# Performance work log

Hardware: AMD Instinct MI355X
Metric: run time of the kernel (lower is better)

The kernel has to match this reference:

```python
import jax, jax.numpy as jnp
import numpy as np

B, S, E, D, V, H, NL = 16, 1024, 64, 256, 10000, 8, 3
HD = D // H


def _ln(x, g, b):
    m = jnp.mean(x, -1, keepdims=True)
    v = jnp.mean((x - m) ** 2, -1, keepdims=True)
    return (x - m) / jnp.sqrt(v + 1e-5) * g + b


def _mha(q_in, kv_in, in_w, in_b, out_w, out_b, causal):
    # torch nn.MultiheadAttention with packed in_proj [3D, D]
    d = q_in.shape[-1]
    q = q_in @ in_w[:d].T + in_b[:d]
    k = kv_in @ in_w[d:2 * d].T + in_b[d:2 * d]
    v = kv_in @ in_w[2 * d:].T + in_b[2 * d:]
    sp = lambda t: t.reshape(t.shape[0], t.shape[1], H, HD).transpose(0, 2, 1, 3)
    q, k, v = sp(q), sp(k), sp(v)
    s = jnp.einsum('bhqd,bhkd->bhqk', q, k) / jnp.float32(np.sqrt(HD))
    if causal:
        L = s.shape[-1]
        s = jnp.where(jnp.tril(jnp.ones((L, L), bool)), s, jnp.float32(-1e30))
    a = jax.nn.softmax(s, -1)
    o = jnp.einsum('bhqk,bhkd->bhqd', a, v).transpose(0, 2, 1, 3).reshape(q_in.shape[0], -1, d)
    return o @ out_w.T + out_b


def setup_inputs() -> dict:
    key = jax.random.key(0)
    ks = iter(jax.random.split(key, 40))
    n = lambda *sh: jax.random.normal(next(ks), sh, jnp.float32) * 0.05
    d = dict(
        tractovka=n(B, E), context=n(B, E), card=n(B, E),
        enc_w=n(3, D, E), enc_b=n(3, D),
        enc_ln_g=jnp.ones((3, D), jnp.float32), enc_ln_b=jnp.zeros((3, D), jnp.float32),
        fusion_w=n(D, 3 * D), fusion_b=n(D),
        fusion_ln_g=jnp.ones(D, jnp.float32), fusion_ln_b=jnp.zeros(D, jnp.float32),
        tok_emb=n(V, D), pos_emb=n(1024, D),
        sa_in_w=n(NL, 3 * D, D), sa_in_b=n(NL, 3 * D), sa_out_w=n(NL, D, D), sa_out_b=n(NL, D),
        ca_in_w=n(NL, 3 * D, D), ca_in_b=n(NL, 3 * D), ca_out_w=n(NL, D, D), ca_out_b=n(NL, D),
        ln1_g=jnp.ones((NL, D), jnp.float32), ln1_b=jnp.zeros((NL, D), jnp.float32),
        ln2_g=jnp.ones((NL, D), jnp.float32), ln2_b=jnp.zeros((NL, D), jnp.float32),
        ln3_g=jnp.ones((NL, D), jnp.float32), ln3_b=jnp.zeros((NL, D), jnp.float32),
        ffn_w1=n(NL, 4 * D, D), ffn_b1=n(NL, 4 * D), ffn_w2=n(NL, D, 4 * D), ffn_b2=n(NL, D),
        out_w=n(V, D), out_b=n(V),
        prev_tokens=jax.random.randint(next(ks), (B, S), 0, V, jnp.int32),
    )
    return d


def reference(tractovka, context, card, enc_w, enc_b, enc_ln_g, enc_ln_b,
              fusion_w, fusion_b, fusion_ln_g, fusion_ln_b, tok_emb, pos_emb,
              sa_in_w, sa_in_b, sa_out_w, sa_out_b, ca_in_w, ca_in_b, ca_out_w, ca_out_b,
              ln1_g, ln1_b, ln2_g, ln2_b, ln3_g, ln3_b,
              ffn_w1, ffn_b1, ffn_w2, ffn_b2, out_w, out_b, prev_tokens):
    enc = lambda x, i: jax.nn.gelu(_ln(x @ enc_w[i].T + enc_b[i], enc_ln_g[i], enc_ln_b[i]), approximate=False)
    mem = jnp.concatenate([enc(tractovka, 0), enc(context, 1), enc(card, 2)], -1)
    mem = jax.nn.gelu(_ln(mem @ fusion_w.T + fusion_b, fusion_ln_g, fusion_ln_b), approximate=False)[:, None, :]  # [B,1,D]
    x = tok_emb[prev_tokens] + pos_emb[:prev_tokens.shape[1]][None]  # [B,S,D]
    for i in range(NL):  # post-norm decoder layer: self-attn, cross-attn, ReLU FFN
        x = _ln(x + _mha(x, x, sa_in_w[i], sa_in_b[i], sa_out_w[i], sa_out_b[i], True), ln1_g[i], ln1_b[i])
        x = _ln(x + _mha(x, mem, ca_in_w[i], ca_in_b[i], ca_out_w[i], ca_out_b[i], False), ln2_g[i], ln2_b[i])
        x = _ln(x + (jax.nn.relu(x @ ffn_w1[i].T + ffn_b1[i]) @ ffn_w2[i].T + ffn_b2[i]), ln3_g[i], ln3_b[i])
    return x @ out_w.T + out_b  # [B,S,V]
```

## Files before the change

### kernel.cpp

```cpp
#include <hip/hip_runtime.h>
#include <math.h>

constexpr int B = 16, S = 1024, D = 256, E = 64, H = 8, HD = 32;

typedef __attribute__((ext_vector_type(8))) short bf16x8;
typedef __attribute__((ext_vector_type(4))) float f32x4;

__device__ __forceinline__ float gelu_f(float x) {
  return 0.5f * x * (1.0f + erff(x * 0.70710678118654752440f));
}

__device__ __forceinline__ unsigned short f2bf(float f) {
  union { float f; unsigned u; } x; x.f = f;
  unsigned r = x.u + 0x7fff + ((x.u >> 16) & 1);
  return (unsigned short)(r >> 16);
}

__device__ __forceinline__ void gl16(const void* g, void* l) {
  __builtin_amdgcn_global_load_lds(
      (const __attribute__((address_space(1))) void*)g,
      (__attribute__((address_space(3))) void*)l, 16, 0, 0);
}

__global__ void k_cvt(const float* __restrict__ src, unsigned short* __restrict__ dst, int n) {
  int i = (blockIdx.x * 256 + threadIdx.x) * 4;
  if (i >= n) return;
  float4 v = *(const float4*)(src + i);
  dst[i + 0] = f2bf(v.x);
  dst[i + 1] = f2bf(v.y);
  dst[i + 2] = f2bf(v.z);
  dst[i + 3] = f2bf(v.w);
}

__global__ void k_embed(const int* __restrict__ tok,
                        const float* __restrict__ tok_emb,
                        const float* __restrict__ pos_emb,
                        float* __restrict__ x, unsigned short* __restrict__ xb) {
  int bs = blockIdx.x;
  int d = threadIdx.x;
  int s = bs & (S - 1);
  int t = tok[bs];
  float v = tok_emb[(size_t)t * D + d] + pos_emb[s * D + d];
  x[(size_t)bs * D + d] = v;
  xb[(size_t)bs * D + d] = f2bf(v);
}

__global__ void k_enc(const float* __restrict__ tr, const float* __restrict__ ctx,
                      const float* __restrict__ card,
                      const float* __restrict__ w, const float* __restrict__ bias,
                      const float* __restrict__ g, const float* __restrict__ bt,
                      float* __restrict__ cat) {
  int b = blockIdx.x, i = blockIdx.y, d = threadIdx.x;
  const float* xin = (i == 0 ? tr : (i == 1 ? ctx : card)) + b * E;
  const float* wr = w + ((size_t)i * D + d) * E;
  float acc = bias[i * D + d];
#pragma unroll 8
  for (int e = 0; e < E; ++e) acc += xin[e] * wr[e];
  __shared__ float s1[D], s2[D];
  s1[d] = acc; s2[d] = acc * acc;
  __syncthreads();
  for (int o = D / 2; o > 0; o >>= 1) {
    if (d < o) { s1[d] += s1[d + o]; s2[d] += s2[d + o]; }
    __syncthreads();
  }
  float mean = s1[0] * (1.0f / D);
  float var = s2[0] * (1.0f / D) - mean * mean;
  float nv = (acc - mean) * rsqrtf(var + 1e-5f) * g[i * D + d] + bt[i * D + d];
  cat[(size_t)b * (3 * D) + i * D + d] = gelu_f(nv);
}

__global__ void k_fusion(const float* __restrict__ cat, const float* __restrict__ w,
                         const float* __restrict__ bias, const float* __restrict__ g,
                         const float* __restrict__ bt, float* __restrict__ mem) {
  int b = blockIdx.x, d = threadIdx.x;
  const float* xr = cat + (size_t)b * (3 * D);
  const float* wr = w + (size_t)d * (3 * D);
  float acc = bias[d];
  for (int k = 0; k < 3 * D; ++k) acc += xr[k] * wr[k];
  __shared__ float s1[D], s2[D];
  s1[d] = acc; s2[d] = acc * acc;
  __syncthreads();
  for (int o = D / 2; o > 0; o >>= 1) {
    if (d < o) { s1[d] += s1[d + o]; s2[d] += s2[d + o]; }
    __syncthreads();
  }
  float mean = s1[0] * (1.0f / D);
  float var = s2[0] * (1.0f / D) - mean * mean;
  float nv = (acc - mean) * rsqrtf(var + 1e-5f) * g[d] + bt[d];
  mem[(size_t)b * D + d] = gelu_f(nv);
}

__global__ void k_ca(const float* __restrict__ mem,
                     const float* __restrict__ in_w, const float* __restrict__ in_b,
                     const float* __restrict__ out_w, const float* __restrict__ out_b,
                     float* __restrict__ ca_add) {
  int b = blockIdx.x, l = blockIdx.y, d = threadIdx.x;
  const float* mr = mem + (size_t)b * D;
  const float* wi = in_w + ((size_t)l * 3 * D + 2 * D + d) * D;
  float v = in_b[(size_t)l * 3 * D + 2 * D + d];
  for (int k = 0; k < D; ++k) v += mr[k] * wi[k];
  __shared__ float vs[D];
  vs[d] = v;
  __syncthreads();
  const float* wo = out_w + ((size_t)l * D + d) * D;
  float o = out_b[(size_t)l * D + d];
  for (int k = 0; k < D; ++k) o += vs[k] * wo[k];
  ca_add[((size_t)l * B + b) * D + d] = o;
}

__global__ __launch_bounds__(256)
void k_attn4(const unsigned short* __restrict__ qkv, unsigned short* __restrict__ out) {
  constexpr int KT = 64;
  __shared__ unsigned short Ks[2][KT * 32];
  __shared__ unsigned short Vt[2][32 * KT];
  __shared__ unsigned short Pl[4 * 32 * KT];

  const int t = threadIdx.x;
  const int w = t >> 6, lane = t & 63;
  const int lg = lane >> 4, lr = lane & 15;
  const int bh = blockIdx.y;
  const int h = bh & (H - 1), b = bh >> 3;
  const int qtile = (int)gridDim.x - 1 - (int)blockIdx.x;
  const int qb = qtile << 7;
  const int qw = qb + w * 32;
  const unsigned short* base = qkv + (size_t)b * S * 768 + h * HD;

  bf16x8 qf[2];
#pragma unroll
  for (int qr = 0; qr < 2; ++qr)
    qf[qr] = *(const bf16x8*)(base + (size_t)(qw + qr * 16 + lr) * 768 + lg * 8);

  f32x4 o[2][2];
#pragma unroll
  for (int qr = 0; qr < 2; ++qr)
#pragma unroll
    for (int dt = 0; dt < 2; ++dt) o[qr][dt] = (f32x4){0.f, 0.f, 0.f, 0.f};
  float mreg[2][4], lreg[2][4];
#pragma unroll
  for (int qr = 0; qr < 2; ++qr)
#pragma unroll
    for (int r = 0; r < 4; ++r) { mreg[qr][r] = -3.0e38f; lreg[qr][r] = 0.f; }

  const float Cs = 0.17677669529663687f * 1.4426950408889634f;

  const int skey = t >> 2;
  const int sch = (t & 3) * 8;
  char* pbase = (char*)Pl + (w << 12);

  const int nkt = (qb + 128) >> 6;

  gl16(base + (size_t)skey * 768 + 256 + sch, (char*)Ks[0] + t * 16);
  bf16x8 vv = *(const bf16x8*)(base + (size_t)skey * 768 + 512 + sch);
  __syncthreads();

  for (int kti = 0; kti < nkt; ++kti) {
    const int kt = kti << 6;
    const int cur = kti & 1;

#pragma unroll
    for (int j = 0; j < 8; ++j) {
      int d = sch + j;
      int byteo = d * (KT * 2) + ((skey * 2) ^ ((d & 7) << 4));
      *(unsigned short*)((char*)Vt[cur] + byteo) = (unsigned short)vv[j];
    }
    if (kti + 1 < nkt) {
      const unsigned short* nb = base + (size_t)(kt + KT + skey) * 768;
      gl16(nb + 256 + sch, (char*)Ks[cur ^ 1] + t * 16);
      vv = *(const bf16x8*)(nb + 512 + sch);
    }

    const bool active = (kt <= qw + 31);
    if (active) {
      bf16x8 kf[4];
#pragma unroll
      for (int t4 = 0; t4 < 4; ++t4)
        kf[t4] = *(const bf16x8*)&Ks[cur][(t4 * 16 + lr) * 32 + lg * 8];
      f32x4 sc[2][4];
#pragma unroll
      for (int qr = 0; qr < 2; ++qr)
#pragma unroll
        for (int t4 = 0; t4 < 4; ++t4)
          sc[qr][t4] = __builtin_amdgcn_mfma_f32_16x16x32_bf16(
              qf[qr], kf[t4], (f32x4){0.f, 0.f, 0.f, 0.f}, 0, 0, 0);

      if (kt + KT > qw) {
#pragma unroll
        for (int qr = 0; qr < 2; ++qr)
#pragma unroll
          for (int t4 = 0; t4 < 4; ++t4)
#pragma unroll
            for (int r = 0; r < 4; ++r) {
              int q = qw + qr * 16 + lg * 4 + r;
              int k = kt + t4 * 16 + lr;
              if (k > q) sc[qr][t4][r] = -3.0e38f;
            }
      }

#pragma unroll
      for (int qr = 0; qr < 2; ++qr) {
#pragma unroll
        for (int r = 0; r < 4; ++r) {
          float mx = fmaxf(fmaxf(sc[qr][0][r], sc[qr][1][r]),
                           fmaxf(sc[qr][2][r], sc[qr][3][r]));
#pragma unroll
          for (int msk = 1; msk <= 8; msk <<= 1) mx = fmaxf(mx, __shfl_xor(mx, msk));
          mx = fmaxf(mx, mreg[qr][r]);
          float cf = exp2f((mreg[qr][r] - mx) * Cs);
          mreg[qr][r] = mx;
          float nmxC = -mx * Cs;
          float ps = 0.f;
#pragma unroll
          for (int t4 = 0; t4 < 4; ++t4) {
            float p = exp2f(fmaf(sc[qr][t4][r], Cs, nmxC));
            sc[qr][t4][r] = p;
            ps += p;
          }
          lreg[qr][r] = lreg[qr][r] * cf + ps;
#pragma unroll
          for (int dt = 0; dt < 2; ++dt) o[qr][dt][r] *= cf;
        }
      }

#pragma unroll
      for (int qr = 0; qr < 2; ++qr)
#pragma unroll
        for (int t4 = 0; t4 < 4; ++t4)
#pragma unroll
          for (int r = 0; r < 4; ++r) {
            int ql = qr * 16 + lg * 4 + r;
            int k = t4 * 16 + lr;
            int byteo = ql * (KT * 2) + ((k * 2) ^ ((ql & 7) << 4));
            *(unsigned short*)(pbase + byteo) = f2bf(sc[qr][t4][r]);
          }
    }

    __syncthreads();

    if (active) {
#pragma unroll
      for (int kp = 0; kp < 2; ++kp) {
        bf16x8 vf[2], pf[2];
        int kb = kp * 64 + lg * 16;
#pragma unroll
        for (int dt = 0; dt < 2; ++dt) {
          int d = dt * 16 + lr;
          vf[dt] = *(const bf16x8*)((char*)Vt[cur] + d * (KT * 2) + (kb ^ ((d & 7) << 4)));
        }
#pragma unroll
        for (int qr = 0; qr < 2; ++qr) {
          int ql = qr * 16 + lr;
          pf[qr] = *(const bf16x8*)(pbase + ql * (KT * 2) + (kb ^ ((ql & 7) << 4)));
        }
#pragma unroll
        for (int qr = 0; qr < 2; ++qr)
#pragma unroll
          for (int dt = 0; dt < 2; ++dt)
            o[qr][dt] = __builtin_amdgcn_mfma_f32_16x16x32_bf16(
                pf[qr], vf[dt], o[qr][dt], 0, 0, 0);
      }
    }
  }

#pragma unroll
  for (int qr = 0; qr < 2; ++qr) {
#pragma unroll
    for (int r = 0; r < 4; ++r) {
      float ls = lreg[qr][r];
#pragma unroll
      for (int msk = 1; msk <= 8; msk <<= 1) ls += __shfl_xor(ls, msk);
      float inv = 1.0f / ls;
      int q = qw + qr * 16 + lg * 4 + r;
      unsigned short* orow = out + (size_t)(b * S + q) * D + h * HD;
#pragma unroll
      for (int dt = 0; dt < 2; ++dt)
        orow[dt * 16 + lr] = f2bf(o[qr][dt][r] * inv);
    }
  }
}

template <int EPI, int OUTBF>
__global__ __launch_bounds__(256)
void k_gemm_mfma(const unsigned short* __restrict__ A,
                 const unsigned short* __restrict__ W,
                 const float* __restrict__ bias,
                 void* __restrict__ Cout,
                 int M, int N, int K) {
  __shared__ unsigned short As[128][32];
  __shared__ unsigned short Bs[128][32];
  int t = threadIdx.x;
  int row0 = blockIdx.y * 128, col0 = blockIdx.x * 128;
  int wid = t >> 6, lane = t & 63;
  int wr = wid >> 1, wc = wid & 1;
  int lrow = lane & 15, lko = (lane >> 4) * 8;

  f32x4 acc[4][4];
#pragma unroll
  for (int mi = 0; mi < 4; ++mi)
#pragma unroll
    for (int ni = 0; ni < 4; ++ni)
      acc[mi][ni] = (f32x4){0.f, 0.f, 0.f, 0.f};

  int c0 = t, c1 = t + 256;
  int ar0 = c0 >> 2, aq0 = (c0 & 3) * 8;
  int ar1 = c1 >> 2, aq1 = (c1 & 3) * 8;
  int wrow0 = col0 + ar0; if (wrow0 > N - 1) wrow0 = N - 1;
  int wrow1 = col0 + ar1; if (wrow1 > N - 1) wrow1 = N - 1;

  const unsigned short* A0 = A + (size_t)(row0 + ar0) * K + aq0;
  const unsigned short* A1 = A + (size_t)(row0 + ar1) * K + aq1;
  const unsigned short* W0 = W + (size_t)wrow0 * K + aq0;
  const unsigned short* W1 = W + (size_t)wrow1 * K + aq1;

  for (int kt = 0; kt < K; kt += 32) {
    gl16(A0 + kt, (char*)As + c0 * 16);
    gl16(A1 + kt, (char*)As + c1 * 16);
    gl16(W0 + kt, (char*)Bs + c0 * 16);
    gl16(W1 + kt, (char*)Bs + c1 * 16);
    __syncthreads();

    bf16x8 af[4], bfr[4];
#pragma unroll
    for (int mi = 0; mi < 4; ++mi)
      af[mi] = *(const bf16x8*)&As[wr * 64 + mi * 16 + lrow][lko];
#pragma unroll
    for (int ni = 0; ni < 4; ++ni)
      bfr[ni] = *(const bf16x8*)&Bs[wc * 64 + ni * 16 + lrow][lko];
#pragma unroll
    for (int mi = 0; mi < 4; ++mi)
#pragma unroll
      for (int ni = 0; ni < 4; ++ni)
        acc[mi][ni] = __builtin_amdgcn_mfma_f32_16x16x32_bf16(af[mi], bfr[ni], acc[mi][ni], 0, 0, 0);
    __syncthreads();
  }

  int rbase = row0 + wr * 64 + (lane >> 4) * 4;
  int cbase = col0 + wc * 64 + lrow;
#pragma unroll
  for (int ni = 0; ni < 4; ++ni) {
    int c = cbase + ni * 16;
    if (c < N) {
      float bv = bias[c];
#pragma unroll
      for (int mi = 0; mi < 4; ++mi) {
        int rr = rbase + mi * 16;
#pragma unroll
        for (int r = 0; r < 4; ++r) {
          float v = acc[mi][ni][r] + bv;
          if (EPI == 1) v = fmaxf(v, 0.0f);
          size_t off = (size_t)(rr + r) * N + c;
          if (OUTBF)
            ((unsigned short*)Cout)[off] = f2bf(v);
          else
            ((float*)Cout)[off] = v;
        }
      }
    }
  }
}

template <int NLN>
__global__ __launch_bounds__(256)
void k_gemm_ln(const unsigned short* __restrict__ A,
               const unsigned short* __restrict__ W,
               const float* __restrict__ bias,
               const float* __restrict__ res,
               const float* __restrict__ ca,
               const float* __restrict__ g1, const float* __restrict__ b1,
               const float* __restrict__ g2, const float* __restrict__ b2,
               float* __restrict__ xout, unsigned short* __restrict__ xb,
               int K) {
  __shared__ unsigned short As[64][32];
  __shared__ unsigned short Bs[256][32];
  __shared__ float red[2][64][4];
  int t = threadIdx.x;
  int row0 = blockIdx.x * 64;
  int wc = t >> 6, lane = t & 63;
  int lr = lane & 15, lg = lane >> 4;

  f32x4 acc[4][4];
#pragma unroll
  for (int mi = 0; mi < 4; ++mi)
#pragma unroll
    for (int ni = 0; ni < 4; ++ni)
      acc[mi][ni] = (f32x4){0.f, 0.f, 0.f, 0.f};

  const unsigned short* srcs[5];
  char* dsts[5];
#pragma unroll
  for (int i = 0; i < 5; ++i) {
    int c = t + (i << 8);
    if (c < 256) {
      int rw = c >> 2, q = (c & 3) * 8;
      srcs[i] = A + (size_t)(row0 + rw) * K + q;
      dsts[i] = (char*)As + c * 16;
    } else {
      int cb = c - 256;
      int rw = cb >> 2, q = (cb & 3) * 8;
      srcs[i] = W + (size_t)rw * K + q;
      dsts[i] = (char*)Bs + cb * 16;
    }
  }

  for (int kt = 0; kt < K; kt += 32) {
#pragma unroll
    for (int i = 0; i < 5; ++i) gl16(srcs[i] + kt, dsts[i]);
    __syncthreads();
    bf16x8 af[4], bfr[4];
#pragma unroll
    for (int mi = 0; mi < 4; ++mi)
      af[mi] = *(const bf16x8*)&As[mi * 16 + lr][lg * 8];
#pragma unroll
    for (int ni = 0; ni < 4; ++ni)
      bfr[ni] = *(const bf16x8*)&Bs[wc * 64 + ni * 16 + lr][lg * 8];
#pragma unroll
    for (int mi = 0; mi < 4; ++mi)
#pragma unroll
      for (int ni = 0; ni < 4; ++ni)
        acc[mi][ni] = __builtin_amdgcn_mfma_f32_16x16x32_bf16(af[mi], bfr[ni], acc[mi][ni], 0, 0, 0);
    __syncthreads();
  }

  int colb = wc * 64 + lr;
  float mean[4][4], rstd[4][4];

#pragma unroll
  for (int mi = 0; mi < 4; ++mi) {
#pragma unroll
    for (int r = 0; r < 4; ++r) {
      int rowl = mi * 16 + lg * 4 + r;
      int rowg = row0 + rowl;
      float s1 = 0.f, s2 = 0.f;
#pragma unroll
      for (int ni = 0; ni < 4; ++ni) {
        int c = colb + ni * 16;
        float v = acc[mi][ni][r] + bias[c] + res[(size_t)rowg * D + c];
        acc[mi][ni][r] = v;
        s1 += v; s2 += v * v;
      }
#pragma unroll
      for (int msk = 1; msk <= 8; msk <<= 1) {
        s1 += __shfl_xor(s1, msk);
        s2 += __shfl_xor(s2, msk);
      }
      if (lr == 0) { red[0][rowl][wc] = s1; red[1][rowl][wc] = s2; }
    }
  }
  __syncthreads();
#pragma unroll
  for (int mi = 0; mi < 4; ++mi)
#pragma unroll
    for (int r = 0; r < 4; ++r) {
      int rowl = mi * 16 + lg * 4 + r;
      f32x4 a = *(const f32x4*)&red[0][rowl][0];
      f32x4 bq = *(const f32x4*)&red[1][rowl][0];
      float s1 = a[0] + a[1] + a[2] + a[3];
      float s2 = bq[0] + bq[1] + bq[2] + bq[3];
      float mn = s1 * (1.0f / D);
      float vr = s2 * (1.0f / D) - mn * mn;
      mean[mi][r] = mn;
      rstd[mi][r] = rsqrtf(vr + 1e-5f);
    }
#pragma unroll
  for (int mi = 0; mi < 4; ++mi)
#pragma unroll
    for (int ni = 0; ni < 4; ++ni) {
      int c = colb + ni * 16;
      float gg = g1[c], bb = b1[c];
#pragma unroll
      for (int r = 0; r < 4; ++r)
        acc[mi][ni][r] = (acc[mi][ni][r] - mean[mi][r]) * rstd[mi][r] * gg + bb;
    }

  if (NLN == 2) {
    __syncthreads();
#pragma unroll
    for (int mi = 0; mi < 4; ++mi) {
#pragma unroll
      for (int r = 0; r < 4; ++r) {
        int rowl = mi * 16 + lg * 4 + r;
        int rowg = row0 + rowl;
        int bidx = rowg >> 10;
        float s1 = 0.f, s2 = 0.f;
#pragma unroll
        for (int ni = 0; ni < 4; ++ni) {
          int c = colb + ni * 16;
          float v = acc[mi][ni][r] + ca[(size_t)bidx * D + c];
          acc[mi][ni][r] = v;
          s1 += v; s2 += v * v;
        }
#pragma unroll
        for (int msk = 1; msk <= 8; msk <<= 1) {
          s1 += __shfl_xor(s1, msk);
          s2 += __shfl_xor(s2, msk);
        }
        if (lr == 0) { red[0][rowl][wc] = s1; red[1][rowl][wc] = s2; }
      }
    }
    __syncthreads();
#pragma unroll
    for (int mi = 0; mi < 4; ++mi)
#pragma unroll
      for (int r = 0; r < 4; ++r) {
        int rowl = mi * 16 + lg * 4 + r;
        f32x4 a = *(const f32x4*)&red[0][rowl][0];
        f32x4 bq = *(const f32x4*)&red[1][rowl][0];
        float s1 = a[0] + a[1] + a[2] + a[3];
        float s2 = bq[0] + bq[1] + bq[2] + bq[3];
        float mn = s1 * (1.0f / D);
        float vr = s2 * (1.0f / D) - mn * mn;
        mean[mi][r] = mn;
        rstd[mi][r] = rsqrtf(vr + 1e-5f);
      }
#pragma unroll
    for (int mi = 0; mi < 4; ++mi)
#pragma unroll
      for (int ni = 0; ni < 4; ++ni) {
        int c = colb + ni * 16;
        float gg = g2[c], bb = b2[c];
#pragma unroll
        for (int r = 0; r < 4; ++r)
          acc[mi][ni][r] = (acc[mi][ni][r] - mean[mi][r]) * rstd[mi][r] * gg + bb;
      }
  }

#pragma unroll
  for (int mi = 0; mi < 4; ++mi)
#pragma unroll
    for (int r = 0; r < 4; ++r) {
      int rowg = row0 + mi * 16 + lg * 4 + r;
#pragma unroll
      for (int ni = 0; ni < 4; ++ni) {
        int c = colb + ni * 16;
        float v = acc[mi][ni][r];
        xout[(size_t)rowg * D + c] = v;
        xb[(size_t)rowg * D + c] = f2bf(v);
      }
    }
}

extern "C" void kernel_launch(void* const* d_in, const int* in_sizes, int n_in,
                              void* d_out, int out_size, void* d_ws, size_t ws_size,
                              hipStream_t stream) {
  (void)in_sizes; (void)n_in; (void)out_size; (void)ws_size;
  const float* tractovka = (const float*)d_in[0];
  const float* context   = (const float*)d_in[1];
  const float* card      = (const float*)d_in[2];
  const float* enc_w     = (const float*)d_in[3];
  const float* enc_b     = (const float*)d_in[4];
  const float* enc_ln_g  = (const float*)d_in[5];
  const float* enc_ln_b  = (const float*)d_in[6];
  const float* fusion_w  = (const float*)d_in[7];
  const float* fusion_b  = (const float*)d_in[8];
  const float* fusion_ln_g = (const float*)d_in[9];
  const float* fusion_ln_b = (const float*)d_in[10];
  const float* tok_emb   = (const float*)d_in[11];
  const float* pos_emb   = (const float*)d_in[12];
  const float* sa_in_w   = (const float*)d_in[13];
  const float* sa_in_b   = (const float*)d_in[14];
  const float* sa_out_w  = (const float*)d_in[15];
  const float* sa_out_b  = (const float*)d_in[16];
  const float* ca_in_w   = (const float*)d_in[17];
  const float* ca_in_b   = (const float*)d_in[18];
  const float* ca_out_w  = (const float*)d_in[19];
  const float* ca_out_b  = (const float*)d_in[20];
  const float* ln1_g     = (const float*)d_in[21];
  const float* ln1_b     = (const float*)d_in[22];
  const float* ln2_g     = (const float*)d_in[23];
  const float* ln2_b     = (const float*)d_in[24];
  const float* ln3_g     = (const float*)d_in[25];
  const float* ln3_b     = (const float*)d_in[26];
  const float* ffn_w1    = (const float*)d_in[27];
  const float* ffn_b1    = (const float*)d_in[28];
  const float* ffn_w2    = (const float*)d_in[29];
  const float* ffn_b2    = (const float*)d_in[30];
  const float* out_w     = (const float*)d_in[31];
  const float* out_b     = (const float*)d_in[32];
  const int*   prev      = (const int*)d_in[33];
  float* out = (float*)d_out;

  const int M = B * S;

  float* ws = (float*)d_ws;
  float* x      = ws;
  float* bufA   = x + (size_t)M * D;
  float* bufB   = bufA + (size_t)M * 768;
  float* cat    = bufB + (size_t)M * D;
  float* mem    = cat + (size_t)B * 3 * D;
  float* ca_add = mem + (size_t)B * D;
  unsigned short* xb    = (unsigned short*)(ca_add + (size_t)3 * B * D);
  unsigned short* attnb = xb + (size_t)M * D;
  unsigned short* wbf   = attnb + (size_t)M * D;
  unsigned short* qkvb  = (unsigned short*)bufA;
  unsigned short* ffn1b = (unsigned short*)bufA;

  const int n_qkvw = 3 * 768 * D;
  const int n_outw = 3 * D * D;
  const int n_f1w  = 3 * 1024 * D;
  const int n_f2w  = 3 * D * 1024;
  const int n_vw   = 10000 * D;
  unsigned short* w_qkv = wbf;
  unsigned short* w_out = w_qkv + n_qkvw;
  unsigned short* w_f1  = w_out + n_outw;
  unsigned short* w_f2  = w_f1 + n_f1w;
  unsigned short* w_v   = w_f2 + n_f2w;

  k_cvt<<<(n_qkvw / 4 + 255) / 256, 256, 0, stream>>>(sa_in_w, w_qkv, n_qkvw);
  k_cvt<<<(n_outw / 4 + 255) / 256, 256, 0, stream>>>(sa_out_w, w_out, n_outw);
  k_cvt<<<(n_f1w / 4 + 255) / 256, 256, 0, stream>>>(ffn_w1, w_f1, n_f1w);
  k_cvt<<<(n_f2w / 4 + 255) / 256, 256, 0, stream>>>(ffn_w2, w_f2, n_f2w);
  k_cvt<<<(n_vw / 4 + 255) / 256, 256, 0, stream>>>(out_w, w_v, n_vw);

  k_embed<<<M, D, 0, stream>>>(prev, tok_emb, pos_emb, x, xb);
  k_enc<<<dim3(B, 3), D, 0, stream>>>(tractovka, context, card, enc_w, enc_b,
                                      enc_ln_g, enc_ln_b, cat);
  k_fusion<<<B, D, 0, stream>>>(cat, fusion_w, fusion_b, fusion_ln_g, fusion_ln_b, mem);
  k_ca<<<dim3(B, 3), D, 0, stream>>>(mem, ca_in_w, ca_in_b, ca_out_w, ca_out_b, ca_add);

  for (int l = 0; l < 3; ++l) {
    k_gemm_mfma<0, 1><<<dim3(6, M / 128), 256, 0, stream>>>(
        xb, w_qkv + (size_t)l * 768 * D, sa_in_b + (size_t)l * 3 * D, qkvb,
        M, 768, D);
    k_attn4<<<dim3(S / 128, B * H), 256, 0, stream>>>(qkvb, attnb);
    k_gemm_ln<2><<<dim3(M / 64), 256, 0, stream>>>(
        attnb, w_out + (size_t)l * D * D, sa_out_b + (size_t)l * D,
        x, ca_add + (size_t)l * B * D,
        ln1_g + (size_t)l * D, ln1_b + (size_t)l * D,
        ln2_g + (size_t)l * D, ln2_b + (size_t)l * D,
        x, xb, D);
    k_gemm_mfma<1, 1><<<dim3(8, M / 128), 256, 0, stream>>>(
        xb, w_f1 + (size_t)l * 1024 * D, ffn_b1 + (size_t)l * 4 * D, ffn1b,
        M, 1024, D);
    k_gemm_ln<1><<<dim3(M / 64), 256, 0, stream>>>(
        ffn1b, w_f2 + (size_t)l * D * 1024, ffn_b2 + (size_t)l * D,
        x, nullptr,
        ln3_g + (size_t)l * D, ln3_b + (size_t)l * D,
        nullptr, nullptr,
        x, xb, 1024);
  }
  k_gemm_mfma<0, 0><<<dim3(79, M / 128), 256, 0, stream>>>(
      xb, w_v, out_b, out, M, 10000, D);
}
```

Measured before the change: 986.7 us.

## Transpose QK^T MFMA so each lane owns one query row in attention

The score MFMA operands are swapped so S^T is computed, which gives each lane one query row across its registers. Row max and sum then need only two cross-lane shuffles instead of four per row, P is packed with v_cvt_pk_bf16 and written as 8-byte stores instead of scalar 2-byte stores, and s_setprio is raised around the MFMA blocks. Rescale factors and the final inverse sum are redistributed to the output layout with __shfl. This aims to cut VALU and LDS-store overhead in the softmax stage, at the cost of extra shuffles for the O rescale.

```diff
diff --git a/kernel.cpp b/kernel.cpp
--- a/kernel.cpp
+++ b/kernel.cpp
@@ -14,6 +14,12 @@
   union { float f; unsigned u; } x; x.f = f;
   unsigned r = x.u + 0x7fff + ((x.u >> 16) & 1);
   return (unsigned short)(r >> 16);
+}
+
+__device__ __forceinline__ unsigned cvt_pk_bf16(float a, float b) {
+  unsigned r;
+  asm("v_cvt_pk_bf16_f32 %0, %1, %2" : "=v"(r) : "v"(a), "v"(b));
+  return r;
 }
 
 __device__ __forceinline__ void gl16(const void* g, void* l) {
@@ -109,7 +115,7 @@
 }
 
 __global__ __launch_bounds__(256)
-void k_attn4(const unsigned short* __restrict__ qkv, unsigned short* __restrict__ out) {
+void k_attn5(const unsigned short* __restrict__ qkv, unsigned short* __restrict__ out) {
   constexpr int KT = 64;
   __shared__ unsigned short Ks[2][KT * 32];
   __shared__ unsigned short Vt[2][32 * KT];
@@ -135,11 +141,9 @@
   for (int qr = 0; qr < 2; ++qr)
 #pragma unroll
     for (int dt = 0; dt < 2; ++dt) o[qr][dt] = (f32x4){0.f, 0.f, 0.f, 0.f};
-  float mreg[2][4], lreg[2][4];
-#pragma unroll
-  for (int qr = 0; qr < 2; ++qr)
-#pragma unroll
-    for (int r = 0; r < 4; ++r) { mreg[qr][r] = -3.0e38f; lreg[qr][r] = 0.f; }
+  float mq[2], lq[2];
+#pragma unroll
+  for (int qr = 0; qr < 2; ++qr) { mq[qr] = -3.0e38f; lq[qr] = 0.f; }
 
   const float Cs = 0.17677669529663687f * 1.4426950408889634f;
 
@@ -176,62 +180,68 @@
       for (int t4 = 0; t4 < 4; ++t4)
         kf[t4] = *(const bf16x8*)&Ks[cur][(t4 * 16 + lr) * 32 + lg * 8];
       f32x4 sc[2][4];
+      __builtin_amdgcn_s_setprio(1);
 #pragma unroll
       for (int qr = 0; qr < 2; ++qr)
 #pragma unroll
         for (int t4 = 0; t4 < 4; ++t4)
           sc[qr][t4] = __builtin_amdgcn_mfma_f32_16x16x32_bf16(
-              qf[qr], kf[t4], (f32x4){0.f, 0.f, 0.f, 0.f}, 0, 0, 0);
+              kf[t4], qf[qr], (f32x4){0.f, 0.f, 0.f, 0.f}, 0, 0, 0);
+      __builtin_amdgcn_s_setprio(0);
 
       if (kt + KT > qw) {
 #pragma unroll
-        for (int qr = 0; qr < 2; ++qr)
+        for (int qr = 0; qr < 2; ++qr) {
+          int q = qw + qr * 16 + lr;
 #pragma unroll
           for (int t4 = 0; t4 < 4; ++t4)
 #pragma unroll
             for (int r = 0; r < 4; ++r) {
-              int q = qw + qr * 16 + lg * 4 + r;
-              int k = kt + t4 * 16 + lr;
+              int k = kt + t4 * 16 + lg * 4 + r;
               if (k > q) sc[qr][t4][r] = -3.0e38f;
             }
+        }
       }
 
 #pragma unroll
       for (int qr = 0; qr < 2; ++qr) {
-#pragma unroll
-        for (int r = 0; r < 4; ++r) {
-          float mx = fmaxf(fmaxf(sc[qr][0][r], sc[qr][1][r]),
-                           fmaxf(sc[qr][2][r], sc[qr][3][r]));
-#pragma unroll
-          for (int msk = 1; msk <= 8; msk <<= 1) mx = fmaxf(mx, __shfl_xor(mx, msk));
-          mx = fmaxf(mx, mreg[qr][r]);
-          float cf = exp2f((mreg[qr][r] - mx) * Cs);
-          mreg[qr][r] = mx;
-          float nmxC = -mx * Cs;
-          float ps = 0.f;
-#pragma unroll
-          for (int t4 = 0; t4 < 4; ++t4) {
+        float mx = sc[qr][0][0];
+#pragma unroll
+        for (int t4 = 0; t4 < 4; ++t4)
+#pragma unroll
+          for (int r = 0; r < 4; ++r) mx = fmaxf(mx, sc[qr][t4][r]);
+        mx = fmaxf(mx, __shfl_xor(mx, 16));
+        mx = fmaxf(mx, __shfl_xor(mx, 32));
+        mx = fmaxf(mx, mq[qr]);
+        float cf = exp2f((mq[qr] - mx) * Cs);
+        mq[qr] = mx;
+        float nmxC = -mx * Cs;
+        float ps = 0.f;
+#pragma unroll
+        for (int t4 = 0; t4 < 4; ++t4)
+#pragma unroll
+          for (int r = 0; r < 4; ++r) {
             float p = exp2f(fmaf(sc[qr][t4][r], Cs, nmxC));
             sc[qr][t4][r] = p;
             ps += p;
           }
-          lreg[qr][r] = lreg[qr][r] * cf + ps;
-#pragma unroll
-          for (int dt = 0; dt < 2; ++dt) o[qr][dt][r] *= cf;
-        }
-      }
-
-#pragma unroll
-      for (int qr = 0; qr < 2; ++qr)
-#pragma unroll
-        for (int t4 = 0; t4 < 4; ++t4)
-#pragma unroll
-          for (int r = 0; r < 4; ++r) {
-            int ql = qr * 16 + lg * 4 + r;
-            int k = t4 * 16 + lr;
-            int byteo = ql * (KT * 2) + ((k * 2) ^ ((ql & 7) << 4));
-            *(unsigned short*)(pbase + byteo) = f2bf(sc[qr][t4][r]);
-          }
+        lq[qr] = lq[qr] * cf + ps;
+#pragma unroll
+        for (int r = 0; r < 4; ++r) {
+          float cfo = __shfl(cf, (lane & 48) | (lg * 4 + r));
+          o[qr][0][r] *= cfo;
+          o[qr][1][r] *= cfo;
+        }
+        int ql = qr * 16 + lr;
+        int swz = (ql & 7) << 4;
+        char* prow = pbase + ql * (KT * 2);
+#pragma unroll
+        for (int t4 = 0; t4 < 4; ++t4) {
+          unsigned lo = cvt_pk_bf16(sc[qr][t4][0], sc[qr][t4][1]);
+          unsigned hi = cvt_pk_bf16(sc[qr][t4][2], sc[qr][t4][3]);
+          *(uint2*)(prow + ((t4 * 32 + lg * 8) ^ swz)) = make_uint2(lo, hi);
+        }
+      }
     }
 
     __syncthreads();
@@ -251,24 +261,27 @@
           int ql = qr * 16 + lr;
           pf[qr] = *(const bf16x8*)(pbase + ql * (KT * 2) + (kb ^ ((ql & 7) << 4)));
         }
+        __builtin_amdgcn_s_setprio(1);
 #pragma unroll
         for (int qr = 0; qr < 2; ++qr)
 #pragma unroll
           for (int dt = 0; dt < 2; ++dt)
             o[qr][dt] = __builtin_amdgcn_mfma_f32_16x16x32_bf16(
                 pf[qr], vf[dt], o[qr][dt], 0, 0, 0);
+        __builtin_amdgcn_s_setprio(0);
       }
     }
   }
 
 #pragma unroll
   for (int qr = 0; qr < 2; ++qr) {
+    float ls = lq[qr];
+    ls += __shfl_xor(ls, 16);
+    ls += __shfl_xor(ls, 32);
+    float invq = 1.0f / ls;
 #pragma unroll
     for (int r = 0; r < 4; ++r) {
-      float ls = lreg[qr][r];
-#pragma unroll
-      for (int msk = 1; msk <= 8; msk <<= 1) ls += __shfl_xor(ls, msk);
-      float inv = 1.0f / ls;
+      float inv = __shfl(invq, (lane & 48) | (lg * 4 + r));
       int q = qw + qr * 16 + lg * 4 + r;
       unsigned short* orow = out + (size_t)(b * S + q) * D + h * HD;
 #pragma unroll
@@ -620,7 +633,7 @@
     k_gemm_mfma<0, 1><<<dim3(6, M / 128), 256, 0, stream>>>(
         xb, w_qkv + (size_t)l * 768 * D, sa_in_b + (size_t)l * 3 * D, qkvb,
         M, 768, D);
-    k_attn4<<<dim3(S / 128, B * H), 256, 0, stream>>>(qkvb, attnb);
+    k_attn5<<<dim3(S / 128, B * H), 256, 0, stream>>>(qkvb, attnb);
     k_gemm_ln<2><<<dim3(M / 64), 256, 0, stream>>>(
         attnb, w_out + (size_t)l * D * D, sa_out_b + (size_t)l * D,
         x, ca_add + (size_t)l * B * D,
```

Measured after the change: 877.4 us. -11.1%, faster.
